# Kernel tuning notes

Hardware: AMD Instinct MI355X
Metric: run time of the kernel (lower is better)

The kernel has to match this reference:

```python
import jax, jax.numpy as jnp
import numpy as np

B, M, N, L = 4096, 128, 96, 20


def setup_inputs() -> dict:
    key = jax.random.key(0)
    k1, k2, k3, k4 = jax.random.split(key, 4)
    x_ini = jax.random.normal(k1, (B, N, 1), jnp.float32)
    y = jax.random.normal(k2, (B, M, 1), jnp.float32)
    H = jax.random.normal(k3, (B, M, N), jnp.float32)
    xt = jax.random.normal(k4, (B, N, 1), jnp.float32)
    # learned parameters, initialized exactly as in the torch __init__
    grad_ss = jnp.full((L,), 0.001, jnp.float32)
    extra = []
    t = 1.0
    for _ in range(L):
        t1 = (1.0 + np.sqrt(1.0 + 4.0 * t * t)) / 2.0
        extra.append((t - 1.0) / t1)
        t = t1
    extra_ss = jnp.asarray(np.array(extra, dtype=np.float32))
    gamma1 = jnp.asarray(np.array([(5.0 - 0.1) / L * i + 0.1 for i in range(L)], dtype=np.float32))
    return {"x_ini": x_ini, "y": y, "H": H, "xt": xt,
            "grad_ss": grad_ss, "extra_ss": extra_ss, "gamma1": gamma1}


def reference(x_ini, y, H, xt, grad_ss, extra_ss, gamma1):
    central = jnp.array([-2.0, 0.0, 2.0], dtype=x_ini.dtype)  # 3-point codebook
    HTH = jnp.einsum('bmn,bmk->bnk', H, H)   # [B,N,N]
    HTy = jnp.einsum('bmn,bmk->bnk', H, y)   # [B,N,1]

    def step(carry, params):
        x, y_x = carry
        gs, es, gm = params
        grad_f = 2.0 * (jnp.matmul(HTH, y_x) - HTy)          # [B,N,1]
        x_buff = y_x - gs * grad_f                            # [B,N,1]
        # nearest-center lookup over the 3-entry codebook
        idx = jnp.argmin(jnp.abs(x_buff - central[None, None, :]), axis=2)  # [B,N]
        center = central[idx][..., None]                      # [B,N,1]
        ply = 2.0 * jax.nn.sigmoid(gm * (x_buff - center)) - 1.0
        y_x_new = ply + es * (ply - x)                        # FISTA momentum
        return (ply, y_x_new), None

    (x, _), _ = jax.lax.scan(step, (x_ini, x_ini), (grad_ss, extra_ss, gamma1))
    d = x - xt
    loss = jnp.sum(d * d).reshape(1, 1)  # sum_b (x-xt)^T (x-xt)
    return x, loss
```

## Files before the change

kernel.cpp:

```cpp
#include <hip/hip_runtime.h>

#define NB 4096
#define MM 128
#define NN 96
#define LL 20

__global__ __launch_bounds__(128)
void pg_kernel(const float* __restrict__ x_ini,
               const float* __restrict__ y,
               const float* __restrict__ H,
               const float* __restrict__ xt,
               const float* __restrict__ grad_ss,
               const float* __restrict__ extra_ss,
               const float* __restrict__ gamma1,
               float* __restrict__ out)
{
    const int b   = blockIdx.x;
    const int tid = threadIdx.x;
    const int cg  = tid & 7;
    const int rg  = tid >> 3;

    __shared__ float lds_wp[16][97];
    __shared__ float lds_yx[96];
    __shared__ float pgs[LL], pes[LL], pgm[LL];
    __shared__ float lsum[2];

    if (tid < LL) {
        pgs[tid] = grad_ss[tid];
        pes[tid] = extra_ss[tid];
        pgm[tid] = gamma1[tid];
    }

    float h[8][12];
    const float* Hb = H + (size_t)b * (MM * NN) + (size_t)(rg * 8) * NN + cg * 12;
    #pragma unroll
    for (int i = 0; i < 8; ++i) {
        #pragma unroll
        for (int k = 0; k < 3; ++k) {
            float4 v = *reinterpret_cast<const float4*>(Hb + i * NN + 4 * k);
            h[i][4*k+0] = v.x; h[i][4*k+1] = v.y;
            h[i][4*k+2] = v.z; h[i][4*k+3] = v.w;
        }
    }

    float yr[8];
    {
        const float* yb = y + (size_t)b * MM + rg * 8;
        float4 v0 = *reinterpret_cast<const float4*>(yb);
        float4 v1 = *reinterpret_cast<const float4*>(yb + 4);
        yr[0]=v0.x; yr[1]=v0.y; yr[2]=v0.z; yr[3]=v0.w;
        yr[4]=v1.x; yr[5]=v1.y; yr[6]=v1.z; yr[7]=v1.w;
    }

    float yx_c = 0.f, x_c = 0.f;
    if (tid < NN) {
        yx_c = x_ini[(size_t)b * NN + tid];
        x_c  = yx_c;
        lds_yx[tid] = yx_c;
    }
    __syncthreads();

    float yx[12];
    #pragma unroll
    for (int k = 0; k < 3; ++k) {
        float4 v = *reinterpret_cast<const float4*>(&lds_yx[cg * 12 + 4 * k]);
        yx[4*k+0]=v.x; yx[4*k+1]=v.y; yx[4*k+2]=v.z; yx[4*k+3]=v.w;
    }

    for (int t = 0; t < LL; ++t) {
        float u[8];
        #pragma unroll
        for (int i = 0; i < 8; ++i) {
            float s = 0.f;
            #pragma unroll
            for (int j = 0; j < 12; ++j) s = fmaf(h[i][j], yx[j], s);
            u[i] = s;
        }
        #pragma unroll
        for (int m = 1; m <= 4; m <<= 1) {
            #pragma unroll
            for (int i = 0; i < 8; ++i) u[i] += __shfl_xor(u[i], m, 64);
        }
        #pragma unroll
        for (int i = 0; i < 8; ++i) u[i] -= yr[i];

        #pragma unroll
        for (int j = 0; j < 12; ++j) {
            float s = 0.f;
            #pragma unroll
            for (int i = 0; i < 8; ++i) s = fmaf(h[i][j], u[i], s);
            lds_wp[rg][cg * 12 + j] = s;
        }
        __syncthreads();

        const float gs = pgs[t], es = pes[t], gm = pgm[t];
        if (tid < NN) {
            float w = 0.f;
            #pragma unroll
            for (int r = 0; r < 16; ++r) w += lds_wp[r][tid];
            float xb  = fmaf(-2.0f * gs, w, yx_c);
            float cen = 2.0f * fminf(fmaxf(rintf(xb * 0.5f), -1.0f), 1.0f);
            float z   = gm * (xb - cen);
            float e   = __expf(-z);
            float ply = fmaf(2.0f, __builtin_amdgcn_rcpf(1.0f + e), -1.0f);
            yx_c = fmaf(es, ply - x_c, ply);
            x_c  = ply;
            lds_yx[tid] = yx_c;
        }
        __syncthreads();

        if (t + 1 < LL) {
            #pragma unroll
            for (int k = 0; k < 3; ++k) {
                float4 v = *reinterpret_cast<const float4*>(&lds_yx[cg * 12 + 4 * k]);
                yx[4*k+0]=v.x; yx[4*k+1]=v.y; yx[4*k+2]=v.z; yx[4*k+3]=v.w;
            }
        }
    }

    float part = 0.f;
    if (tid < NN) {
        out[(size_t)b * NN + tid] = x_c;
        float d = x_c - xt[(size_t)b * NN + tid];
        part = d * d;
    }
    #pragma unroll
    for (int m = 1; m < 64; m <<= 1) part += __shfl_xor(part, m, 64);
    if ((tid & 63) == 0) lsum[tid >> 6] = part;
    __syncthreads();
    if (tid == 0) atomicAdd(out + (size_t)NB * NN, lsum[0] + lsum[1]);
}

extern "C" void kernel_launch(void* const* d_in, const int* in_sizes, int n_in,
                              void* d_out, int out_size, void* d_ws, size_t ws_size,
                              hipStream_t stream) {
    const float* x_ini   = (const float*)d_in[0];
    const float* y       = (const float*)d_in[1];
    const float* H       = (const float*)d_in[2];
    const float* xt      = (const float*)d_in[3];
    const float* grad_ss = (const float*)d_in[4];
    const float* extra_ss= (const float*)d_in[5];
    const float* gamma1  = (const float*)d_in[6];
    float* out = (float*)d_out;

    hipMemsetAsync(out + (size_t)NB * NN, 0, sizeof(float), stream);

    pg_kernel<<<NB, 128, 0, stream>>>(x_ini, y, H, xt,
                                      grad_ss, extra_ss, gamma1, out);
}
```

Baseline: 107.8 us.

## Precompute H^T H and H^T y with split-bf16 MFMA, iterate on Gram matrix

Replaces the per-iteration two-pass H*x / H^T*u matvecs with a one-time Gram matrix H^T[H|y] built on MFMA units, using a hi/lo bf16 split with three products to approximate fp32 accuracy. Each of the 20 iterations then does a single 96-length dot product per thread against its own Gram row held in registers, with a double-buffered LDS y_x vector and one barrier per step. This trades the repeated streaming of H from registers for a larger up-front matmul, heavy register use (96-float rows), and some precision loss from the bf16 split.

```diff
diff --git a/kernel.cpp b/kernel.cpp
--- a/kernel.cpp
+++ b/kernel.cpp
@@ -5,7 +5,22 @@
 #define NN 96
 #define LL 20
 
-__global__ __launch_bounds__(128)
+typedef __attribute__((ext_vector_type(8))) short bf16x8;
+typedef __attribute__((ext_vector_type(4)))  float f32x4;
+
+#define HT_HI      0
+#define HT_LO      18432
+#define HT_STRIDE  144
+#define HTH_OFF    0
+#define HTH_STRIDE 400
+#define U_SIZE     38400
+
+__device__ __forceinline__ unsigned bf16_rne(float f) {
+    unsigned u = __float_as_uint(f);
+    return (u + 0x7fffu + ((u >> 16) & 1u)) >> 16;
+}
+
+__global__ __launch_bounds__(128, 2)
 void pg_kernel(const float* __restrict__ x_ini,
                const float* __restrict__ y,
                const float* __restrict__ H,
@@ -15,107 +30,149 @@
                const float* __restrict__ gamma1,
                float* __restrict__ out)
 {
-    const int b   = blockIdx.x;
-    const int tid = threadIdx.x;
-    const int cg  = tid & 7;
-    const int rg  = tid >> 3;
-
-    __shared__ float lds_wp[16][97];
-    __shared__ float lds_yx[96];
+    __shared__ __align__(16) char U[U_SIZE];
+    __shared__ __align__(16) float yxbuf[2][NN];
     __shared__ float pgs[LL], pes[LL], pgm[LL];
     __shared__ float lsum[2];
 
-    if (tid < LL) {
-        pgs[tid] = grad_ss[tid];
-        pes[tid] = extra_ss[tid];
-        pgm[tid] = gamma1[tid];
-    }
-
-    float h[8][12];
-    const float* Hb = H + (size_t)b * (MM * NN) + (size_t)(rg * 8) * NN + cg * 12;
+    const int b    = blockIdx.x;
+    const int tid  = threadIdx.x;
+    const int lane = tid & 63;
+    const int wid  = tid >> 6;
+
+    if (tid < LL) { pgs[tid] = grad_ss[tid]; pes[tid] = extra_ss[tid]; pgm[tid] = gamma1[tid]; }
+
+    f32x4 acc[3][7];
     #pragma unroll
-    for (int i = 0; i < 8; ++i) {
-        #pragma unroll
-        for (int k = 0; k < 3; ++k) {
-            float4 v = *reinterpret_cast<const float4*>(Hb + i * NN + 4 * k);
-            h[i][4*k+0] = v.x; h[i][4*k+1] = v.y;
-            h[i][4*k+2] = v.z; h[i][4*k+3] = v.w;
-        }
-    }
-
-    float yr[8];
-    {
-        const float* yb = y + (size_t)b * MM + rg * 8;
-        float4 v0 = *reinterpret_cast<const float4*>(yb);
-        float4 v1 = *reinterpret_cast<const float4*>(yb + 4);
-        yr[0]=v0.x; yr[1]=v0.y; yr[2]=v0.z; yr[3]=v0.w;
-        yr[4]=v1.x; yr[5]=v1.y; yr[6]=v1.z; yr[7]=v1.w;
-    }
-
-    float yx_c = 0.f, x_c = 0.f;
+    for (int i = 0; i < 3; ++i)
+        #pragma unroll
+        for (int j = 0; j < 7; ++j)
+            #pragma unroll
+            for (int r = 0; r < 4; ++r) acc[i][j][r] = 0.f;
+
+    const int c32 = tid & 31;
+    const int ko  = tid >> 5;
+    const float* Hb = H + (size_t)b * (MM * NN);
+
+    for (int kh = 0; kh < 2; ++kh) {
+        if (kh) __syncthreads();
+
+        #pragma unroll
+        for (int cg = 0; cg < 3; ++cg) {
+            const int c = c32 + 32 * cg;
+            float v[16];
+            #pragma unroll
+            for (int rr = 0; rr < 16; ++rr)
+                v[rr] = Hb[(size_t)(kh * 64 + ko * 16 + rr) * NN + c];
+            bf16x8 h0, h1, l0, l1;
+            #pragma unroll
+            for (int j = 0; j < 8; ++j) {
+                unsigned ha = bf16_rne(v[j]);
+                unsigned hb = bf16_rne(v[8 + j]);
+                h0[j] = (short)ha;
+                h1[j] = (short)hb;
+                l0[j] = (short)bf16_rne(v[j]     - __uint_as_float(ha << 16));
+                l1[j] = (short)bf16_rne(v[8 + j] - __uint_as_float(hb << 16));
+            }
+            char* ph = &U[HT_HI + c * HT_STRIDE + ko * 32];
+            char* pl = &U[HT_LO + c * HT_STRIDE + ko * 32];
+            *(bf16x8*)(ph)      = h0;
+            *(bf16x8*)(ph + 16) = h1;
+            *(bf16x8*)(pl)      = l0;
+            *(bf16x8*)(pl + 16) = l1;
+        }
+        if (tid < 64) {
+            float vy = y[(size_t)b * MM + kh * 64 + tid];
+            unsigned hb = bf16_rne(vy);
+            float lo = vy - __uint_as_float(hb << 16);
+            *(unsigned short*)&U[HT_HI + 96 * HT_STRIDE + tid * 2] = (unsigned short)hb;
+            *(unsigned short*)&U[HT_LO + 96 * HT_STRIDE + tid * 2] = (unsigned short)bf16_rne(lo);
+        }
+        __syncthreads();
+
+        #pragma unroll
+        for (int kk = 0; kk < 2; ++kk) {
+            const int kb = kk * 64 + (lane >> 4) * 16;
+            bf16x8 Ah[3], Al[3], Bh[7], Bl[7];
+            #pragma unroll
+            for (int i = 0; i < 3; ++i) {
+                const int off = (wid * 48 + i * 16 + (lane & 15)) * HT_STRIDE + kb;
+                Ah[i] = *(const bf16x8*)&U[HT_HI + off];
+                Al[i] = *(const bf16x8*)&U[HT_LO + off];
+            }
+            #pragma unroll
+            for (int j = 0; j < 7; ++j) {
+                const int off = (j * 16 + (lane & 15)) * HT_STRIDE + kb;
+                Bh[j] = *(const bf16x8*)&U[HT_HI + off];
+                Bl[j] = *(const bf16x8*)&U[HT_LO + off];
+            }
+            #pragma unroll
+            for (int i = 0; i < 3; ++i)
+                #pragma unroll
+                for (int j = 0; j < 7; ++j) {
+                    acc[i][j] = __builtin_amdgcn_mfma_f32_16x16x32_bf16(Ah[i], Bh[j], acc[i][j], 0, 0, 0);
+                    acc[i][j] = __builtin_amdgcn_mfma_f32_16x16x32_bf16(Ah[i], Bl[j], acc[i][j], 0, 0, 0);
+                    acc[i][j] = __builtin_amdgcn_mfma_f32_16x16x32_bf16(Al[i], Bh[j], acc[i][j], 0, 0, 0);
+                }
+        }
+    }
+    __syncthreads();
+
+    #pragma unroll
+    for (int i = 0; i < 3; ++i)
+        #pragma unroll
+        for (int j = 0; j < 7; ++j) {
+            const int col = j * 16 + (lane & 15);
+            if (col < 97) {
+                const int rowb = wid * 48 + i * 16 + (lane >> 4) * 4;
+                #pragma unroll
+                for (int r = 0; r < 4; ++r)
+                    *(float*)&U[HTH_OFF + (rowb + r) * HTH_STRIDE + col * 4] = acc[i][j][r];
+            }
+        }
+    __syncthreads();
+
+    float hrow[96];
+    float hty = 0.f, yx_own = 0.f, x_c = 0.f;
     if (tid < NN) {
-        yx_c = x_ini[(size_t)b * NN + tid];
-        x_c  = yx_c;
-        lds_yx[tid] = yx_c;
-    }
-    __syncthreads();
-
-    float yx[12];
-    #pragma unroll
-    for (int k = 0; k < 3; ++k) {
-        float4 v = *reinterpret_cast<const float4*>(&lds_yx[cg * 12 + 4 * k]);
-        yx[4*k+0]=v.x; yx[4*k+1]=v.y; yx[4*k+2]=v.z; yx[4*k+3]=v.w;
-    }
-
+        #pragma unroll
+        for (int g = 0; g < 24; ++g) {
+            float4 v = *(const float4*)&U[HTH_OFF + tid * HTH_STRIDE + 16 * g];
+            hrow[4*g+0] = v.x; hrow[4*g+1] = v.y; hrow[4*g+2] = v.z; hrow[4*g+3] = v.w;
+        }
+        hty    = *(const float*)&U[HTH_OFF + tid * HTH_STRIDE + 96 * 4];
+        yx_own = x_ini[(size_t)b * NN + tid];
+        x_c    = yx_own;
+        yxbuf[0][tid] = yx_own;
+    }
+    __syncthreads();
+
+    int cur = 0;
     for (int t = 0; t < LL; ++t) {
-        float u[8];
-        #pragma unroll
-        for (int i = 0; i < 8; ++i) {
-            float s = 0.f;
-            #pragma unroll
-            for (int j = 0; j < 12; ++j) s = fmaf(h[i][j], yx[j], s);
-            u[i] = s;
-        }
-        #pragma unroll
-        for (int m = 1; m <= 4; m <<= 1) {
-            #pragma unroll
-            for (int i = 0; i < 8; ++i) u[i] += __shfl_xor(u[i], m, 64);
-        }
-        #pragma unroll
-        for (int i = 0; i < 8; ++i) u[i] -= yr[i];
-
-        #pragma unroll
-        for (int j = 0; j < 12; ++j) {
-            float s = 0.f;
-            #pragma unroll
-            for (int i = 0; i < 8; ++i) s = fmaf(h[i][j], u[i], s);
-            lds_wp[rg][cg * 12 + j] = s;
-        }
-        __syncthreads();
-
-        const float gs = pgs[t], es = pes[t], gm = pgm[t];
         if (tid < NN) {
-            float w = 0.f;
-            #pragma unroll
-            for (int r = 0; r < 16; ++r) w += lds_wp[r][tid];
-            float xb  = fmaf(-2.0f * gs, w, yx_c);
+            float w0 = 0.f, w1 = 0.f, w2 = 0.f, w3 = 0.f;
+            #pragma unroll
+            for (int g = 0; g < 24; ++g) {
+                float4 v = *(const float4*)&yxbuf[cur][4 * g];
+                w0 = fmaf(hrow[4*g+0], v.x, w0);
+                w1 = fmaf(hrow[4*g+1], v.y, w1);
+                w2 = fmaf(hrow[4*g+2], v.z, w2);
+                w3 = fmaf(hrow[4*g+3], v.w, w3);
+            }
+            float w = (w0 + w1) + (w2 + w3);
+            const float gs = pgs[t], es = pes[t], gm = pgm[t];
+            float xb  = fmaf(-2.0f * gs, w - hty, yx_own);
             float cen = 2.0f * fminf(fmaxf(rintf(xb * 0.5f), -1.0f), 1.0f);
             float z   = gm * (xb - cen);
             float e   = __expf(-z);
             float ply = fmaf(2.0f, __builtin_amdgcn_rcpf(1.0f + e), -1.0f);
-            yx_c = fmaf(es, ply - x_c, ply);
-            x_c  = ply;
-            lds_yx[tid] = yx_c;
-        }
+            float yxn = fmaf(es, ply - x_c, ply);
+            x_c    = ply;
+            yx_own = yxn;
+            yxbuf[cur ^ 1][tid] = yxn;
+        }
+        cur ^= 1;
         __syncthreads();
-
-        if (t + 1 < LL) {
-            #pragma unroll
-            for (int k = 0; k < 3; ++k) {
-                float4 v = *reinterpret_cast<const float4*>(&lds_yx[cg * 12 + 4 * k]);
-                yx[4*k+0]=v.x; yx[4*k+1]=v.y; yx[4*k+2]=v.z; yx[4*k+3]=v.w;
-            }
-        }
     }
 
     float part = 0.f;
@@ -134,17 +191,15 @@
 extern "C" void kernel_launch(void* const* d_in, const int* in_sizes, int n_in,
                               void* d_out, int out_size, void* d_ws, size_t ws_size,
                               hipStream_t stream) {
-    const float* x_ini   = (const float*)d_in[0];
-    const float* y       = (const float*)d_in[1];
-    const float* H       = (const float*)d_in[2];
-    const float* xt      = (const float*)d_in[3];
-    const float* grad_ss = (const float*)d_in[4];
-    const float* extra_ss= (const float*)d_in[5];
-    const float* gamma1  = (const float*)d_in[6];
+    const float* x_ini    = (const float*)d_in[0];
+    const float* y        = (const float*)d_in[1];
+    const float* H        = (const float*)d_in[2];
+    const float* xt       = (const float*)d_in[3];
+    const float* grad_ss  = (const float*)d_in[4];
+    const float* extra_ss = (const float*)d_in[5];
+    const float* gamma1   = (const float*)d_in[6];
     float* out = (float*)d_out;
 
     hipMemsetAsync(out + (size_t)NB * NN, 0, sizeof(float), stream);
-
-    pg_kernel<<<NB, 128, 0, stream>>>(x_ini, y, H, xt,
-                                      grad_ss, extra_ss, gamma1, out);
+    pg_kernel<<<NB, 128, 0, stream>>>(x_ini, y, H, xt, grad_ss, extra_ss, gamma1, out);
 }
```

Result: slower. 127.6 us, median of 2 (+18.4%).

## Split each batch item across 256 threads with 4 H rows per thread

Applied to the files above, without the earlier changes.

Doubles the block size from 128 to 256 threads so each thread holds 4 rows by 12 columns of H in registers instead of 8 by 12. This roughly halves the per-thread FMA chain each iteration and lowers register pressure to allow more waves per CU. The partial-sum buffer grows to 32 rows and is written with float4 stores. The column reduction is split across four accumulators. An extra barrier per iteration is added so the yx vector can be reused safely. The cost is a longer 32-row cross-thread reduction, done by only 96 threads, and more barriers per step.

```diff
diff --git a/kernel.cpp b/kernel.cpp
--- a/kernel.cpp
+++ b/kernel.cpp
@@ -5,7 +5,7 @@
 #define NN 96
 #define LL 20
 
-__global__ __launch_bounds__(128)
+__global__ __launch_bounds__(256, 2)
 void pg_kernel(const float* __restrict__ x_ini,
                const float* __restrict__ y,
                const float* __restrict__ H,
@@ -20,21 +20,17 @@
     const int cg  = tid & 7;
     const int rg  = tid >> 3;
 
-    __shared__ float lds_wp[16][97];
-    __shared__ float lds_yx[96];
+    __shared__ __align__(16) float wp[32][100];
+    __shared__ __align__(16) float yxb[NN];
     __shared__ float pgs[LL], pes[LL], pgm[LL];
-    __shared__ float lsum[2];
+    __shared__ float lsum[4];
 
-    if (tid < LL) {
-        pgs[tid] = grad_ss[tid];
-        pes[tid] = extra_ss[tid];
-        pgm[tid] = gamma1[tid];
-    }
+    if (tid < LL) { pgs[tid] = grad_ss[tid]; pes[tid] = extra_ss[tid]; pgm[tid] = gamma1[tid]; }
 
-    float h[8][12];
-    const float* Hb = H + (size_t)b * (MM * NN) + (size_t)(rg * 8) * NN + cg * 12;
+    float h[4][12];
+    const float* Hb = H + (size_t)b * (MM * NN) + (size_t)(rg * 4) * NN + cg * 12;
     #pragma unroll
-    for (int i = 0; i < 8; ++i) {
+    for (int i = 0; i < 4; ++i) {
         #pragma unroll
         for (int k = 0; k < 3; ++k) {
             float4 v = *reinterpret_cast<const float4*>(Hb + i * NN + 4 * k);
@@ -43,34 +39,31 @@
         }
     }
 
-    float yr[8];
+    float yr[4];
     {
-        const float* yb = y + (size_t)b * MM + rg * 8;
-        float4 v0 = *reinterpret_cast<const float4*>(yb);
-        float4 v1 = *reinterpret_cast<const float4*>(yb + 4);
-        yr[0]=v0.x; yr[1]=v0.y; yr[2]=v0.z; yr[3]=v0.w;
-        yr[4]=v1.x; yr[5]=v1.y; yr[6]=v1.z; yr[7]=v1.w;
+        float4 v = *reinterpret_cast<const float4*>(y + (size_t)b * MM + rg * 4);
+        yr[0] = v.x; yr[1] = v.y; yr[2] = v.z; yr[3] = v.w;
     }
 
-    float yx_c = 0.f, x_c = 0.f;
+    float yx_own = 0.f, x_c = 0.f;
     if (tid < NN) {
-        yx_c = x_ini[(size_t)b * NN + tid];
-        x_c  = yx_c;
-        lds_yx[tid] = yx_c;
+        yx_own = x_ini[(size_t)b * NN + tid];
+        x_c    = yx_own;
+        yxb[tid] = yx_own;
     }
     __syncthreads();
 
     float yx[12];
     #pragma unroll
     for (int k = 0; k < 3; ++k) {
-        float4 v = *reinterpret_cast<const float4*>(&lds_yx[cg * 12 + 4 * k]);
+        float4 v = *reinterpret_cast<const float4*>(&yxb[cg * 12 + 4 * k]);
         yx[4*k+0]=v.x; yx[4*k+1]=v.y; yx[4*k+2]=v.z; yx[4*k+3]=v.w;
     }
 
     for (int t = 0; t < LL; ++t) {
-        float u[8];
+        float u[4];
         #pragma unroll
-        for (int i = 0; i < 8; ++i) {
+        for (int i = 0; i < 4; ++i) {
             float s = 0.f;
             #pragma unroll
             for (int j = 0; j < 12; ++j) s = fmaf(h[i][j], yx[j], s);
@@ -79,42 +72,50 @@
         #pragma unroll
         for (int m = 1; m <= 4; m <<= 1) {
             #pragma unroll
-            for (int i = 0; i < 8; ++i) u[i] += __shfl_xor(u[i], m, 64);
+            for (int i = 0; i < 4; ++i) u[i] += __shfl_xor(u[i], m, 64);
         }
         #pragma unroll
-        for (int i = 0; i < 8; ++i) u[i] -= yr[i];
+        for (int i = 0; i < 4; ++i) u[i] -= yr[i];
 
         #pragma unroll
-        for (int j = 0; j < 12; ++j) {
-            float s = 0.f;
-            #pragma unroll
-            for (int i = 0; i < 8; ++i) s = fmaf(h[i][j], u[i], s);
-            lds_wp[rg][cg * 12 + j] = s;
+        for (int k = 0; k < 3; ++k) {
+            float4 s;
+            s.x = fmaf(h[0][4*k+0], u[0], fmaf(h[1][4*k+0], u[1], fmaf(h[2][4*k+0], u[2], h[3][4*k+0] * u[3])));
+            s.y = fmaf(h[0][4*k+1], u[0], fmaf(h[1][4*k+1], u[1], fmaf(h[2][4*k+1], u[2], h[3][4*k+1] * u[3])));
+            s.z = fmaf(h[0][4*k+2], u[0], fmaf(h[1][4*k+2], u[1], fmaf(h[2][4*k+2], u[2], h[3][4*k+2] * u[3])));
+            s.w = fmaf(h[0][4*k+3], u[0], fmaf(h[1][4*k+3], u[1], fmaf(h[2][4*k+3], u[2], h[3][4*k+3] * u[3])));
+            *reinterpret_cast<float4*>(&wp[rg][cg * 12 + 4 * k]) = s;
         }
         __syncthreads();
 
-        const float gs = pgs[t], es = pes[t], gm = pgm[t];
         if (tid < NN) {
-            float w = 0.f;
+            float a0 = 0.f, a1 = 0.f, a2 = 0.f, a3 = 0.f;
             #pragma unroll
-            for (int r = 0; r < 16; ++r) w += lds_wp[r][tid];
-            float xb  = fmaf(-2.0f * gs, w, yx_c);
+            for (int r = 0; r < 8; ++r) {
+                a0 += wp[4*r+0][tid];
+                a1 += wp[4*r+1][tid];
+                a2 += wp[4*r+2][tid];
+                a3 += wp[4*r+3][tid];
+            }
+            float w = (a0 + a1) + (a2 + a3);
+            const float gs = pgs[t], es = pes[t], gm = pgm[t];
+            float xb  = fmaf(-2.0f * gs, w, yx_own);
             float cen = 2.0f * fminf(fmaxf(rintf(xb * 0.5f), -1.0f), 1.0f);
             float z   = gm * (xb - cen);
             float e   = __expf(-z);
             float ply = fmaf(2.0f, __builtin_amdgcn_rcpf(1.0f + e), -1.0f);
-            yx_c = fmaf(es, ply - x_c, ply);
-            x_c  = ply;
-            lds_yx[tid] = yx_c;
+            yx_own = fmaf(es, ply - x_c, ply);
+            x_c    = ply;
+            if (t + 1 < LL) yxb[tid] = yx_own;
         }
-        __syncthreads();
-
         if (t + 1 < LL) {
+            __syncthreads();
             #pragma unroll
             for (int k = 0; k < 3; ++k) {
-                float4 v = *reinterpret_cast<const float4*>(&lds_yx[cg * 12 + 4 * k]);
+                float4 v = *reinterpret_cast<const float4*>(&yxb[cg * 12 + 4 * k]);
                 yx[4*k+0]=v.x; yx[4*k+1]=v.y; yx[4*k+2]=v.z; yx[4*k+3]=v.w;
             }
+            __syncthreads();
         }
     }
 
@@ -128,23 +129,21 @@
     for (int m = 1; m < 64; m <<= 1) part += __shfl_xor(part, m, 64);
     if ((tid & 63) == 0) lsum[tid >> 6] = part;
     __syncthreads();
-    if (tid == 0) atomicAdd(out + (size_t)NB * NN, lsum[0] + lsum[1]);
+    if (tid == 0) atomicAdd(out + (size_t)NB * NN, (lsum[0] + lsum[1]) + (lsum[2] + lsum[3]));
 }
 
 extern "C" void kernel_launch(void* const* d_in, const int* in_sizes, int n_in,
                               void* d_out, int out_size, void* d_ws, size_t ws_size,
                               hipStream_t stream) {
-    const float* x_ini   = (const float*)d_in[0];
-    const float* y       = (const float*)d_in[1];
-    const float* H       = (const float*)d_in[2];
-    const float* xt      = (const float*)d_in[3];
-    const float* grad_ss = (const float*)d_in[4];
-    const float* extra_ss= (const float*)d_in[5];
-    const float* gamma1  = (const float*)d_in[6];
+    const float* x_ini    = (const float*)d_in[0];
+    const float* y        = (const float*)d_in[1];
+    const float* H        = (const float*)d_in[2];
+    const float* xt       = (const float*)d_in[3];
+    const float* grad_ss  = (const float*)d_in[4];
+    const float* extra_ss = (const float*)d_in[5];
+    const float* gamma1   = (const float*)d_in[6];
     float* out = (float*)d_out;
 
     hipMemsetAsync(out + (size_t)NB * NN, 0, sizeof(float), stream);
-
-    pg_kernel<<<NB, 128, 0, stream>>>(x_ini, y, H, xt,
-                                      grad_ss, extra_ss, gamma1, out);
+    pg_kernel<<<NB, 256, 0, stream>>>(x_ini, y, H, xt, grad_ss, extra_ss, gamma1, out);
 }
```

After: 124.1 us. 1.15x slower.
